# Optimization experiments

Measured on AMD Instinct MI355X. Metric: run time of the kernel, lower is better.

The kernel has to match this reference:

```python
import jax, jax.numpy as jnp
import numpy as np

DIM_MODEL = 1024
N_HEAD = 16
N_HEAD_H = 16
DIM_KEY = 64
DIM_VALUE = 64


def _linear_params(key, out_f, in_f):
    kw, kb = jax.random.split(key)
    bound = 1.0 / np.sqrt(in_f)
    W = jax.random.uniform(kw, (out_f, in_f), jnp.float32, -bound, bound)
    b = jax.random.uniform(kb, (out_f,), jnp.float32, -bound, bound)
    return W, b


def setup_inputs() -> dict:
    key = jax.random.key(0)
    ks = jax.random.split(key, 12)
    B, L = 4, 1024
    queries = jax.random.normal(ks[0], (B, L, DIM_MODEL), jnp.float32)
    keys = jax.random.normal(ks[1], (B, L, DIM_MODEL), jnp.float32)
    values = jax.random.normal(ks[2], (B, L, DIM_MODEL), jnp.float32)
    mask = jnp.ones((B, L), dtype=jnp.bool_)  # accepted but unused by the module
    attn_bias = jax.random.normal(ks[3], (B, N_HEAD, L), jnp.float32)
    Wq, bq = _linear_params(ks[4], DIM_KEY * N_HEAD, DIM_MODEL)
    Wk, bk = _linear_params(ks[5], DIM_KEY * N_HEAD, DIM_MODEL)
    Wv, bv = _linear_params(ks[6], DIM_VALUE * N_HEAD, DIM_MODEL)
    Wl, bl = _linear_params(ks[7], N_HEAD_H, N_HEAD)
    Ww, bw = _linear_params(ks[8], N_HEAD, N_HEAD_H)
    Wo, bo = _linear_params(ks[9], DIM_MODEL, DIM_VALUE * N_HEAD)
    return {
        "queries": queries, "keys": keys, "values": values,
        "mask": mask, "attn_bias": attn_bias,
        "Wq": Wq, "bq": bq, "Wk": Wk, "bk": bk, "Wv": Wv, "bv": bv,
        "Wl": Wl, "bl": bl, "Ww": Ww, "bw": bw, "Wo": Wo, "bo": bo,
    }


def reference(queries, keys, values, mask, attn_bias,
              Wq, bq, Wk, bk, Wv, bv, Wl, bl, Ww, bw, Wo, bo):
    B, Lq, _ = queries.shape
    # projections -> [B, L, H, d]
    q = (queries @ Wq.T + bq).reshape(B, Lq, N_HEAD, DIM_KEY)
    k = (keys @ Wk.T + bk).reshape(B, keys.shape[1], N_HEAD, DIM_KEY)
    v = (values @ Wv.T + bv).reshape(B, values.shape[1], N_HEAD, DIM_VALUE)
    scale = DIM_KEY ** (-0.5)
    # scores in the module's [B, Lq, Lk, H] layout (after its two transposes)
    scores = jnp.einsum("bqhd,bkhd->bqkh", scale * q, k)
    # attn_bias [B, H, Lq] -> [B, Lq, 1, H], broadcast over Lk
    scores = scores + jnp.transpose(attn_bias, (0, 2, 1))[:, :, None, :]
    # pre-softmax head mixing (fc_l): [B, Lq, Lk, H] -> [B, Lq, Lk, Hh]
    logits = jnp.einsum("bqkh,gh->bqkg", scores, Wl) + bl
    weights = jax.nn.softmax(logits, axis=2)  # softmax over Lk
    # post-softmax head mixing (fc_w): [B, Lq, Lk, Hh] -> [B, Lq, Lk, H]
    weights = jnp.einsum("bqkg,hg->bqkh", weights, Ww) + bw
    # weighted values: [B, Lq, H, dv] -> combine heads -> fc_o
    ctx = jnp.einsum("bqkh,bkhd->bqhd", weights, v).reshape(B, Lq, N_HEAD * DIM_VALUE)
    return ctx @ Wo.T + bo
```

## Files before the change

kernel.cpp:

```cpp
#include <hip/hip_runtime.h>

#define L_ 1024
#define DM 1024

typedef float f32x4 __attribute__((ext_vector_type(4)));
typedef _Float16 f16;
typedef _Float16 f16x8 __attribute__((ext_vector_type(8)));
typedef _Float16 f16x4 __attribute__((ext_vector_type(4)));

__device__ __forceinline__ void gload16(const void* g, void* l) {
  __builtin_amdgcn_global_load_lds(
      (const __attribute__((address_space(1))) unsigned int*)g,
      (__attribute__((address_space(3))) unsigned int*)l, 16, 0, 0);
}

__global__ __launch_bounds__(256) void cvt_all(const float* __restrict__ q,
    const float* __restrict__ k, const float* __restrict__ v,
    const float* __restrict__ wq, const float* __restrict__ wk,
    const float* __restrict__ wv, const float* __restrict__ wo,
    f16* __restrict__ dbig, f16* __restrict__ dw, f16* __restrict__ dwo) {
  int i = blockIdx.x * 256 + threadIdx.x;
  const float* s; f16* d; int off;
  if (i < 524288)       { s = q;  d = dbig;           off = i; }
  else if (i < 1048576) { s = k;  d = dbig + 4194304; off = i - 524288; }
  else if (i < 1572864) { s = v;  d = dbig + 8388608; off = i - 1048576; }
  else if (i < 1703936) { s = wq; d = dw;             off = i - 1572864; }
  else if (i < 1835008) { s = wk; d = dw + 1048576;   off = i - 1703936; }
  else if (i < 1966080) { s = wv; d = dw + 2097152;   off = i - 1835008; }
  else                  { s = wo; d = dwo;            off = i - 1966080; }
  const float4* sp = (const float4*)s + (size_t)off * 2;
  float4 a = sp[0], bb = sp[1];
  f16x8 o;
  o[0] = (f16)a.x;  o[1] = (f16)a.y;  o[2] = (f16)a.z;  o[3] = (f16)a.w;
  o[4] = (f16)bb.x; o[5] = (f16)bb.y; o[6] = (f16)bb.z; o[7] = (f16)bb.w;
  ((f16x8*)d)[off] = o;
}

__global__ __launch_bounds__(256) void biascat(const float* __restrict__ bq,
    const float* __restrict__ bk, const float* __restrict__ bv, float* __restrict__ o) {
  int t = blockIdx.x * 256 + threadIdx.x;
  o[t] = (t < 1024) ? bq[t] : (t < 2048) ? bk[t - 1024] : bv[t - 2048];
}

__global__ __launch_bounds__(256) void proj_gemm(const f16* __restrict__ Ain,
    const f16* __restrict__ Wc, const float* __restrict__ bcat, f16* __restrict__ QKVp) {
  alignas(16) __shared__ f16 At0[128 * 32];
  alignas(16) __shared__ f16 At1[128 * 32];
  alignas(16) __shared__ f16 Bt0[64 * 32];
  alignas(16) __shared__ f16 Bt1[64 * 32];
  int z = blockIdx.z;
  const f16* A = Ain + (size_t)z * 4194304;
  const f16* W = Wc + (size_t)z * 1048576;
  int t = threadIdx.x, lane = t & 63;
  int w = t >> 6, wr = w >> 1, wc = w & 1;
  int bid = blockIdx.x;
  int xcd = bid & 7, local = bid >> 3;
  int bm = (xcd * 4 + (local >> 4)) * 128;
  int bn = (local & 15) * 64;
  f32x4 acc[4][2] = {};
  int rbA = 32 * w + (lane >> 2);
  int rbB = 16 * w + (lane >> 2);
  int c8 = (lane & 3) * 8;
  const f16* gA = A + (size_t)(bm + rbA) * 1024 + c8;
  const f16* gB = W + (size_t)(bn + rbB) * 1024 + c8;
  f16* lA00 = &At0[(2 * w) * 512];      f16* lA01 = &At0[(2 * w + 1) * 512];
  f16* lA10 = &At1[(2 * w) * 512];      f16* lA11 = &At1[(2 * w + 1) * 512];
  f16* lB0  = &Bt0[w * 512];            f16* lB1  = &Bt1[w * 512];
  int ro = (lane & 15) * 32 + (lane >> 4) * 8;
  for (int kk = 0; kk < 1024; kk += 64) {
    gload16(gA + kk, lA00);
    gload16(gA + 16 * 1024 + kk, lA01);
    gload16(gA + kk + 32, lA10);
    gload16(gA + 16 * 1024 + kk + 32, lA11);
    gload16(gB + kk, lB0);
    gload16(gB + kk + 32, lB1);
    __syncthreads();
    f16x8 af[4], af2[4], bf[2], bf2[2];
    #pragma unroll
    for (int m = 0; m < 4; ++m) {
      af[m]  = *(const f16x8*)&At0[(wr * 64 + m * 16) * 32 + ro];
      af2[m] = *(const f16x8*)&At1[(wr * 64 + m * 16) * 32 + ro];
    }
    #pragma unroll
    for (int n = 0; n < 2; ++n) {
      bf[n]  = *(const f16x8*)&Bt0[(wc * 32 + n * 16) * 32 + ro];
      bf2[n] = *(const f16x8*)&Bt1[(wc * 32 + n * 16) * 32 + ro];
    }
    #pragma unroll
    for (int m = 0; m < 4; ++m)
      #pragma unroll
      for (int n = 0; n < 2; ++n) {
        acc[m][n] = __builtin_amdgcn_mfma_f32_16x16x32_f16(af[m], bf[n], acc[m][n], 0, 0, 0);
        acc[m][n] = __builtin_amdgcn_mfma_f32_16x16x32_f16(af2[m], bf2[n], acc[m][n], 0, 0, 0);
      }
    __syncthreads();
  }
  float scale = (z == 0) ? 0.125f : 1.0f;
  #pragma unroll
  for (int n = 0; n < 2; ++n) {
    int cn = bn + wc * 32 + n * 16 + (lane & 15);
    float bvv = bcat[z * 1024 + cn];
    #pragma unroll
    for (int m = 0; m < 4; ++m) {
      int r0 = bm + wr * 64 + m * 16 + (lane >> 4) * 4;
      #pragma unroll
      for (int r = 0; r < 4; ++r)
        QKVp[(size_t)(r0 + r) * 3072 + z * 1024 + cn] = (f16)((acc[m][n][r] + bvv) * scale);
    }
  }
}

__global__ __launch_bounds__(256) void gemm_out(const f16* __restrict__ A,
    const f16* __restrict__ W, const float* __restrict__ bias, float* __restrict__ C) {
  alignas(16) __shared__ f16 At0[128 * 32];
  alignas(16) __shared__ f16 At1[128 * 32];
  alignas(16) __shared__ f16 Bt0[64 * 32];
  alignas(16) __shared__ f16 Bt1[64 * 32];
  int t = threadIdx.x, lane = t & 63;
  int w = t >> 6, wr = w >> 1, wc = w & 1;
  int bid = blockIdx.x;
  int xcd = bid & 7, local = bid >> 3;
  int bm = (xcd * 4 + (local >> 4)) * 128;
  int bn = (local & 15) * 64;
  f32x4 acc[4][2] = {};
  int rbA = 32 * w + (lane >> 2);
  int rbB = 16 * w + (lane >> 2);
  int c8 = (lane & 3) * 8;
  const f16* gA = A + (size_t)(bm + rbA) * 1024 + c8;
  const f16* gB = W + (size_t)(bn + rbB) * 1024 + c8;
  f16* lA00 = &At0[(2 * w) * 512];      f16* lA01 = &At0[(2 * w + 1) * 512];
  f16* lA10 = &At1[(2 * w) * 512];      f16* lA11 = &At1[(2 * w + 1) * 512];
  f16* lB0  = &Bt0[w * 512];            f16* lB1  = &Bt1[w * 512];
  int ro = (lane & 15) * 32 + (lane >> 4) * 8;
  for (int kk = 0; kk < 1024; kk += 64) {
    gload16(gA + kk, lA00);
    gload16(gA + 16 * 1024 + kk, lA01);
    gload16(gA + kk + 32, lA10);
    gload16(gA + 16 * 1024 + kk + 32, lA11);
    gload16(gB + kk, lB0);
    gload16(gB + kk + 32, lB1);
    __syncthreads();
    f16x8 af[4], af2[4], bf[2], bf2[2];
    #pragma unroll
    for (int m = 0; m < 4; ++m) {
      af[m]  = *(const f16x8*)&At0[(wr * 64 + m * 16) * 32 + ro];
      af2[m] = *(const f16x8*)&At1[(wr * 64 + m * 16) * 32 + ro];
    }
    #pragma unroll
    for (int n = 0; n < 2; ++n) {
      bf[n]  = *(const f16x8*)&Bt0[(wc * 32 + n * 16) * 32 + ro];
      bf2[n] = *(const f16x8*)&Bt1[(wc * 32 + n * 16) * 32 + ro];
    }
    #pragma unroll
    for (int m = 0; m < 4; ++m)
      #pragma unroll
      for (int n = 0; n < 2; ++n) {
        acc[m][n] = __builtin_amdgcn_mfma_f32_16x16x32_f16(af[m], bf[n], acc[m][n], 0, 0, 0);
        acc[m][n] = __builtin_amdgcn_mfma_f32_16x16x32_f16(af2[m], bf2[n], acc[m][n], 0, 0, 0);
      }
    __syncthreads();
  }
  #pragma unroll
  for (int n = 0; n < 2; ++n) {
    int cn = bn + wc * 32 + n * 16 + (lane & 15);
    float bvv = bias[cn];
    #pragma unroll
    for (int m = 0; m < 4; ++m) {
      int r0 = bm + wr * 64 + m * 16 + (lane >> 4) * 4;
      #pragma unroll
      for (int r = 0; r < 4; ++r)
        C[(size_t)(r0 + r) * 1024 + cn] = acc[m][n][r] + bvv;
    }
  }
}

__global__ __launch_bounds__(256) void transpose_v(const f16* __restrict__ QKVp,
                                                   f16* __restrict__ Vt) {
  alignas(16) __shared__ f16 T[64 * 72];
  int bh = blockIdx.y;
  int b = bh >> 4, h = bh & 15;
  int kt = blockIdx.x;
  int t = threadIdx.x;
  int krow = t >> 2, part = t & 3;
  const f16x8* src = (const f16x8*)(QKVp + (size_t)(b * L_ + kt * 64 + krow) * 3072 + 2048 + h * 64 + part * 16);
  f16x8 v0 = src[0], v1 = src[1];
  *(f16x8*)&T[krow * 72 + part * 16] = v0;
  *(f16x8*)&T[krow * 72 + part * 16 + 8] = v1;
  __syncthreads();
  int drow = t >> 2;
  f16x8 o0, o1;
  #pragma unroll
  for (int j = 0; j < 8; ++j) o0[j] = T[(part * 16 + j) * 72 + drow];
  #pragma unroll
  for (int j = 0; j < 8; ++j) o1[j] = T[(part * 16 + 8 + j) * 72 + drow];
  f16* dst = Vt + (size_t)(bh * 64 + drow) * L_ + kt * 64 + part * 16;
  *(f16x8*)dst = o0;
  *(f16x8*)(dst + 8) = o1;
}

__global__ __launch_bounds__(256) void cbias_kernel(const float* __restrict__ ab,
    const float* __restrict__ Wl, const float* __restrict__ bl, float* __restrict__ cb) {
  int t = blockIdx.x * 256 + threadIdx.x;
  int b = t >> 14, q = (t >> 4) & 1023, g = t & 15;
  float s = bl[g];
  #pragma unroll
  for (int h = 0; h < 16; ++h) s += ab[(size_t)(b * 16 + h) * L_ + q] * Wl[g * 16 + h];
  cb[t] = s;
}

__global__ __launch_bounds__(256) void qk_gemm(const f16* __restrict__ QKVp,
                                               f16* __restrict__ S, int b0) {
  alignas(16) __shared__ f16 At[128 * 72];
  alignas(16) __shared__ f16 Bt[128 * 72];
  int t = threadIdx.x, lane = t & 63;
  int wid = t >> 6, wr = wid >> 1, wc = wid & 1;
  int kt = blockIdx.x, qt = blockIdx.y;
  int h = blockIdx.z & 15, bz = blockIdx.z >> 4;
  int b = b0 + bz;
  #pragma unroll
  for (int i = 0; i < 4; ++i) {
    int row = i * 32 + (t >> 3), c = (t & 7) * 8;
    *(f16x8*)&At[row * 72 + c] =
        *(const f16x8*)(QKVp + (size_t)(b * 1024 + qt * 128 + row) * 3072 + h * 64 + c);
    *(f16x8*)&Bt[row * 72 + c] =
        *(const f16x8*)(QKVp + (size_t)(b * 1024 + kt * 128 + row) * 3072 + 1024 + h * 64 + c);
  }
  __syncthreads();
  int l15 = lane & 15, lhi = lane >> 4;
  f32x4 acc[4][4] = {};
  #pragma unroll
  for (int s = 0; s < 2; ++s) {
    f16x8 af[4], bf[4];
    #pragma unroll
    for (int m = 0; m < 4; ++m) af[m] = *(const f16x8*)&At[(wr * 64 + m * 16 + l15) * 72 + s * 32 + lhi * 8];
    #pragma unroll
    for (int n = 0; n < 4; ++n) bf[n] = *(const f16x8*)&Bt[(wc * 64 + n * 16 + l15) * 72 + s * 32 + lhi * 8];
    #pragma unroll
    for (int m = 0; m < 4; ++m)
      #pragma unroll
      for (int n = 0; n < 4; ++n)
        acc[m][n] = __builtin_amdgcn_mfma_f32_16x16x32_f16(af[m], bf[n], acc[m][n], 0, 0, 0);
  }
  size_t Sh = (size_t)(bz * 16 + h) * 1048576;
  #pragma unroll
  for (int n = 0; n < 4; ++n) {
    int col = kt * 128 + wc * 64 + n * 16 + l15;
    #pragma unroll
    for (int m = 0; m < 4; ++m) {
      int q0 = qt * 128 + wr * 64 + m * 16 + lhi * 4;
      #pragma unroll
      for (int r = 0; r < 4; ++r)
        S[Sh + (size_t)(q0 + r) * 1024 + col] = (f16)acc[m][n][r];
    }
  }
}

__global__ __launch_bounds__(256) void msm_kernel(f16* __restrict__ S,
    const float* __restrict__ Wl, const float* __restrict__ Ww,
    const float* __restrict__ bwv, const float* __restrict__ cb, int b0) {
  alignas(16) __shared__ f16 Sl[16][1032];
  __shared__ float red[4][16];
  __shared__ float rlv16[16];
  int t = threadIdx.x;
  int q = blockIdx.x & 1023, bz = blockIdx.x >> 10;
  int lane = t & 63, w = t >> 6, l15 = lane & 15, lhi = lane >> 4;
  size_t Sq = (size_t)(bz * 16) * 1048576 + (size_t)q * 1024;
  #pragma unroll
  for (int i = 0; i < 8; ++i) {
    int idx = i * 256 + t, h = idx >> 7, c = (idx & 127) * 8;
    *(f16x8*)&Sl[h][c] = *(const f16x8*)(S + Sq + (size_t)h * 1048576 + c);
  }
  f16x4 b1;
  #pragma unroll
  for (int j = 0; j < 4; ++j) b1[j] = (f16)Wl[l15 * 16 + lhi * 4 + j];
  float cbv = cb[((size_t)((b0 + bz) * 1024 + q)) * 16 + l15];
  __syncthreads();
  float dsum = 0.f;
  for (int i = 0; i < 16; ++i) {
    int kt = w * 16 + i;
    int krow = kt * 16 + l15;
    f16x4 a1;
    #pragma unroll
    for (int j = 0; j < 4; ++j) a1[j] = Sl[lhi * 4 + j][krow];
    f32x4 d = __builtin_amdgcn_mfma_f32_16x16x16f16(a1, b1, (f32x4){0.f, 0.f, 0.f, 0.f}, 0, 0, 0);
    int k0 = kt * 16 + lhi * 4;
    f16x4 ev;
    #pragma unroll
    for (int r = 0; r < 4; ++r) {
      float e = __expf(d[r] + cbv);
      dsum += e;
      ev[r] = (f16)e;
    }
    *(f16x4*)&Sl[l15][k0] = ev;
  }
  dsum += __shfl_xor(dsum, 16);
  dsum += __shfl_xor(dsum, 32);
  if (lane < 16) red[w][lane] = dsum;
  __syncthreads();
  if (t < 16) rlv16[t] = 1.0f / (red[0][t] + red[1][t] + red[2][t] + red[3][t]);
  __syncthreads();
  f16x4 b2;
  #pragma unroll
  for (int j = 0; j < 4; ++j) b2[j] = (f16)(Ww[l15 * 16 + lhi * 4 + j] * rlv16[lhi * 4 + j]);
  float bwh = bwv[l15];
  for (int i = 0; i < 16; ++i) {
    int kt = w * 16 + i;
    int krow = kt * 16 + l15;
    f16x4 a2;
    #pragma unroll
    for (int j = 0; j < 4; ++j) a2[j] = Sl[lhi * 4 + j][krow];
    f32x4 d = __builtin_amdgcn_mfma_f32_16x16x16f16(a2, b2, (f32x4){0.f, 0.f, 0.f, 0.f}, 0, 0, 0);
    int k0 = kt * 16 + lhi * 4;
    f16x4 wv4;
    #pragma unroll
    for (int r = 0; r < 4; ++r) wv4[r] = (f16)(d[r] + bwh);
    *(f16x4*)&Sl[l15][k0] = wv4;
  }
  __syncthreads();
  #pragma unroll
  for (int i = 0; i < 8; ++i) {
    int idx = i * 256 + t, h = idx >> 7, c = (idx & 127) * 8;
    *(f16x8*)(S + Sq + (size_t)h * 1048576 + c) = *(f16x8*)&Sl[h][c];
  }
}

__global__ __launch_bounds__(256) void pv_gemm(const f16* __restrict__ Sw,
    const f16* __restrict__ Vt, f16* __restrict__ ctx, int b0) {
  alignas(16) __shared__ f16 Aw[32 * 72];
  alignas(16) __shared__ f16 Bv[64 * 72];
  int t = threadIdx.x, lane = t & 63, w = t >> 6;
  int qt = blockIdx.x, h = blockIdx.y, bz = blockIdx.z;
  int wr = w >> 1, wc = w & 1;
  int l15 = lane & 15, lhi = lane >> 4;
  const f16* Sh = Sw + (size_t)(bz * 16 + h) * 1048576 + (size_t)(qt * 32) * 1024;
  const f16* Vh = Vt + (size_t)((b0 + bz) * 16 + h) * 64 * 1024;
  f32x4 acc[2] = {};
  int srow = t >> 3, scol = (t & 7) * 8;
  for (int kk = 0; kk < 1024; kk += 64) {
    __syncthreads();
    *(f16x8*)&Aw[srow * 72 + scol] = *(const f16x8*)(Sh + (size_t)srow * 1024 + kk + scol);
    *(f16x8*)&Bv[srow * 72 + scol] = *(const f16x8*)(Vh + (size_t)srow * 1024 + kk + scol);
    *(f16x8*)&Bv[(srow + 32) * 72 + scol] = *(const f16x8*)(Vh + (size_t)(srow + 32) * 1024 + kk + scol);
    __syncthreads();
    #pragma unroll
    for (int s = 0; s < 2; ++s) {
      f16x8 af = *(const f16x8*)&Aw[(wr * 16 + l15) * 72 + s * 32 + lhi * 8];
      #pragma unroll
      for (int n = 0; n < 2; ++n) {
        f16x8 bf = *(const f16x8*)&Bv[(wc * 32 + n * 16 + l15) * 72 + s * 32 + lhi * 8];
        acc[n] = __builtin_amdgcn_mfma_f32_16x16x32_f16(af, bf, acc[n], 0, 0, 0);
      }
    }
  }
  #pragma unroll
  for (int n = 0; n < 2; ++n) {
    int col = h * 64 + wc * 32 + n * 16 + l15;
    int q0 = (b0 + bz) * 1024 + qt * 32 + wr * 16 + lhi * 4;
    #pragma unroll
    for (int r = 0; r < 4; ++r)
      ctx[(size_t)(q0 + r) * 1024 + col] = (f16)acc[n][r];
  }
}

extern "C" void kernel_launch(void* const* d_in, const int* in_sizes, int n_in,
                              void* d_out, int out_size, void* d_ws, size_t ws_size,
                              hipStream_t stream) {
  const float* queries = (const float*)d_in[0];
  const float* keys    = (const float*)d_in[1];
  const float* values  = (const float*)d_in[2];
  const float* ab  = (const float*)d_in[4];
  const float* Wq  = (const float*)d_in[5];  const float* bq = (const float*)d_in[6];
  const float* Wk  = (const float*)d_in[7];  const float* bk = (const float*)d_in[8];
  const float* Wv  = (const float*)d_in[9];  const float* bv = (const float*)d_in[10];
  const float* Wl  = (const float*)d_in[11]; const float* bl = (const float*)d_in[12];
  const float* Ww  = (const float*)d_in[13]; const float* bwp = (const float*)d_in[14];
  const float* Wo  = (const float*)d_in[15]; const float* bo = (const float*)d_in[16];

  char* ws = (char*)d_ws;
  const size_t MB = 1024 * 1024;
  bool full = ws_size >= 172 * MB;

  f16* qin   = (f16*)(ws + 0 * MB);
  f16* wqkv  = (f16*)(ws + 24 * MB);
  f16* S     = (f16*)(ws + 0 * MB);
  f16* QKVp  = (f16*)(ws + (full ? 128 : 32) * MB);
  f16* Vt    = (f16*)(ws + (full ? 152 : 56) * MB);
  float* cbp = (float*)(ws + (full ? 170 : 64) * MB);
  f16* wo16  = (f16*)(ws + (full ? 168 : 65) * MB);
  f16* ctx   = (f16*)(ws + (full ? 160 : 67) * MB);
  float* bqkv = (float*)(ws + (full ? 170 * MB + 512 * 1024 : 30 * MB));

  cvt_all<<<8192, 256, 0, stream>>>(queries, keys, values, Wq, Wk, Wv, Wo, qin, wqkv, wo16);
  biascat<<<12, 256, 0, stream>>>(bq, bk, bv, bqkv);
  proj_gemm<<<dim3(512, 1, 3), 256, 0, stream>>>(qin, wqkv, bqkv, QKVp);
  transpose_v<<<dim3(16, 64), 256, 0, stream>>>(QKVp, Vt);
  cbias_kernel<<<256, 256, 0, stream>>>(ab, Wl, bl, cbp);

  if (full) {
    qk_gemm<<<dim3(8, 8, 64), 256, 0, stream>>>(QKVp, S, 0);
    msm_kernel<<<4096, 256, 0, stream>>>(S, Wl, Ww, bwp, cbp, 0);
    pv_gemm<<<dim3(32, 16, 4), 256, 0, stream>>>(S, Vt, ctx, 0);
  } else {
    for (int b = 0; b < 4; ++b) {
      qk_gemm<<<dim3(8, 8, 16), 256, 0, stream>>>(QKVp, S, b);
      msm_kernel<<<1024, 256, 0, stream>>>(S, Wl, Ww, bwp, cbp, b);
      pv_gemm<<<dim3(32, 16, 1), 256, 0, stream>>>(S, Vt, ctx, b);
    }
  }

  gemm_out<<<dim3(512), 256, 0, stream>>>(ctx, wo16, bo, (float*)d_out);
}
```

Baseline: 196.4 us.

## Fuse fp32-to-fp16 activation conversion into the QKV projection GEMM

The standalone conversion of the query/key/value activations to fp16 is removed. The projection GEMM now reads the fp32 activations directly, converts them in registers and stores them into a padded LDS tile (row stride 36). This drops a full write and re-read of 24 MB of fp16 activations plus most of the conversion launch. In exchange each GEMM block reads twice the bytes per A tile through synchronous vector loads instead of async global-to-LDS loads, and those A loads are re-read by the 16 column blocks.

```diff
diff --git a/kernel.cpp b/kernel.cpp
--- a/kernel.cpp
+++ b/kernel.cpp
@@ -14,20 +14,15 @@
       (__attribute__((address_space(3))) unsigned int*)l, 16, 0, 0);
 }
 
-__global__ __launch_bounds__(256) void cvt_all(const float* __restrict__ q,
-    const float* __restrict__ k, const float* __restrict__ v,
-    const float* __restrict__ wq, const float* __restrict__ wk,
-    const float* __restrict__ wv, const float* __restrict__ wo,
-    f16* __restrict__ dbig, f16* __restrict__ dw, f16* __restrict__ dwo) {
+__global__ __launch_bounds__(256) void cvt_w(const float* __restrict__ wq,
+    const float* __restrict__ wk, const float* __restrict__ wv, const float* __restrict__ wo,
+    f16* __restrict__ dw, f16* __restrict__ dwo) {
   int i = blockIdx.x * 256 + threadIdx.x;
   const float* s; f16* d; int off;
-  if (i < 524288)       { s = q;  d = dbig;           off = i; }
-  else if (i < 1048576) { s = k;  d = dbig + 4194304; off = i - 524288; }
-  else if (i < 1572864) { s = v;  d = dbig + 8388608; off = i - 1048576; }
-  else if (i < 1703936) { s = wq; d = dw;             off = i - 1572864; }
-  else if (i < 1835008) { s = wk; d = dw + 1048576;   off = i - 1703936; }
-  else if (i < 1966080) { s = wv; d = dw + 2097152;   off = i - 1835008; }
-  else                  { s = wo; d = dwo;            off = i - 1966080; }
+  if (i < 131072)       { s = wq; d = dw;             off = i; }
+  else if (i < 262144)  { s = wk; d = dw + 1048576;   off = i - 131072; }
+  else if (i < 393216)  { s = wv; d = dw + 2097152;   off = i - 262144; }
+  else                  { s = wo; d = dwo;            off = i - 393216; }
   const float4* sp = (const float4*)s + (size_t)off * 2;
   float4 a = sp[0], bb = sp[1];
   f16x8 o;
@@ -42,14 +37,15 @@
   o[t] = (t < 1024) ? bq[t] : (t < 2048) ? bk[t - 1024] : bv[t - 2048];
 }
 
-__global__ __launch_bounds__(256) void proj_gemm(const f16* __restrict__ Ain,
+__global__ __launch_bounds__(256) void proj_gemm(const float* __restrict__ Aq,
+    const float* __restrict__ Ak, const float* __restrict__ Av,
     const f16* __restrict__ Wc, const float* __restrict__ bcat, f16* __restrict__ QKVp) {
-  alignas(16) __shared__ f16 At0[128 * 32];
-  alignas(16) __shared__ f16 At1[128 * 32];
+  alignas(16) __shared__ f16 At0[128 * 36];
+  alignas(16) __shared__ f16 At1[128 * 36];
   alignas(16) __shared__ f16 Bt0[64 * 32];
   alignas(16) __shared__ f16 Bt1[64 * 32];
   int z = blockIdx.z;
-  const f16* A = Ain + (size_t)z * 4194304;
+  const float* A = (z == 0) ? Aq : (z == 1) ? Ak : Av;
   const f16* W = Wc + (size_t)z * 1048576;
   int t = threadIdx.x, lane = t & 63;
   int w = t >> 6, wr = w >> 1, wc = w & 1;
@@ -58,33 +54,46 @@
   int bm = (xcd * 4 + (local >> 4)) * 128;
   int bn = (local & 15) * 64;
   f32x4 acc[4][2] = {};
-  int rbA = 32 * w + (lane >> 2);
+  int arow = t >> 1, ahalf = t & 1;
+  const float4* gA = (const float4*)(A + (size_t)(bm + arow) * 1024 + ahalf * 32);
+  f16* aDst = (ahalf ? At1 : At0) + arow * 36;
   int rbB = 16 * w + (lane >> 2);
   int c8 = (lane & 3) * 8;
-  const f16* gA = A + (size_t)(bm + rbA) * 1024 + c8;
   const f16* gB = W + (size_t)(bn + rbB) * 1024 + c8;
-  f16* lA00 = &At0[(2 * w) * 512];      f16* lA01 = &At0[(2 * w + 1) * 512];
-  f16* lA10 = &At1[(2 * w) * 512];      f16* lA11 = &At1[(2 * w + 1) * 512];
-  f16* lB0  = &Bt0[w * 512];            f16* lB1  = &Bt1[w * 512];
-  int ro = (lane & 15) * 32 + (lane >> 4) * 8;
+  f16* lB0 = &Bt0[w * 512];
+  f16* lB1 = &Bt1[w * 512];
+  int roA = (lane & 15) * 36 + (lane >> 4) * 8;
+  int roB = (lane & 15) * 32 + (lane >> 4) * 8;
   for (int kk = 0; kk < 1024; kk += 64) {
-    gload16(gA + kk, lA00);
-    gload16(gA + 16 * 1024 + kk, lA01);
-    gload16(gA + kk + 32, lA10);
-    gload16(gA + 16 * 1024 + kk + 32, lA11);
     gload16(gB + kk, lB0);
     gload16(gB + kk + 32, lB1);
+    const float4* ga = gA + (kk >> 2);
+    float4 v0 = ga[0], v1 = ga[1], v2 = ga[2], v3 = ga[3];
+    float4 v4 = ga[4], v5 = ga[5], v6 = ga[6], v7 = ga[7];
+    f16x8 o0, o1, o2, o3;
+    o0[0] = (f16)v0.x; o0[1] = (f16)v0.y; o0[2] = (f16)v0.z; o0[3] = (f16)v0.w;
+    o0[4] = (f16)v1.x; o0[5] = (f16)v1.y; o0[6] = (f16)v1.z; o0[7] = (f16)v1.w;
+    o1[0] = (f16)v2.x; o1[1] = (f16)v2.y; o1[2] = (f16)v2.z; o1[3] = (f16)v2.w;
+    o1[4] = (f16)v3.x; o1[5] = (f16)v3.y; o1[6] = (f16)v3.z; o1[7] = (f16)v3.w;
+    o2[0] = (f16)v4.x; o2[1] = (f16)v4.y; o2[2] = (f16)v4.z; o2[3] = (f16)v4.w;
+    o2[4] = (f16)v5.x; o2[5] = (f16)v5.y; o2[6] = (f16)v5.z; o2[7] = (f16)v5.w;
+    o3[0] = (f16)v6.x; o3[1] = (f16)v6.y; o3[2] = (f16)v6.z; o3[3] = (f16)v6.w;
+    o3[4] = (f16)v7.x; o3[5] = (f16)v7.y; o3[6] = (f16)v7.z; o3[7] = (f16)v7.w;
+    *(f16x8*)&aDst[0]  = o0;
+    *(f16x8*)&aDst[8]  = o1;
+    *(f16x8*)&aDst[16] = o2;
+    *(f16x8*)&aDst[24] = o3;
     __syncthreads();
     f16x8 af[4], af2[4], bf[2], bf2[2];
     #pragma unroll
     for (int m = 0; m < 4; ++m) {
-      af[m]  = *(const f16x8*)&At0[(wr * 64 + m * 16) * 32 + ro];
-      af2[m] = *(const f16x8*)&At1[(wr * 64 + m * 16) * 32 + ro];
+      af[m]  = *(const f16x8*)&At0[(wr * 64 + m * 16) * 36 + roA];
+      af2[m] = *(const f16x8*)&At1[(wr * 64 + m * 16) * 36 + roA];
     }
     #pragma unroll
     for (int n = 0; n < 2; ++n) {
-      bf[n]  = *(const f16x8*)&Bt0[(wc * 32 + n * 16) * 32 + ro];
-      bf2[n] = *(const f16x8*)&Bt1[(wc * 32 + n * 16) * 32 + ro];
+      bf[n]  = *(const f16x8*)&Bt0[(wc * 32 + n * 16) * 32 + roB];
+      bf2[n] = *(const f16x8*)&Bt1[(wc * 32 + n * 16) * 32 + roB];
     }
     #pragma unroll
     for (int m = 0; m < 4; ++m)
@@ -380,7 +389,6 @@
   const size_t MB = 1024 * 1024;
   bool full = ws_size >= 172 * MB;
 
-  f16* qin   = (f16*)(ws + 0 * MB);
   f16* wqkv  = (f16*)(ws + 24 * MB);
   f16* S     = (f16*)(ws + 0 * MB);
   f16* QKVp  = (f16*)(ws + (full ? 128 : 32) * MB);
@@ -390,9 +398,9 @@
   f16* ctx   = (f16*)(ws + (full ? 160 : 67) * MB);
   float* bqkv = (float*)(ws + (full ? 170 * MB + 512 * 1024 : 30 * MB));
 
-  cvt_all<<<8192, 256, 0, stream>>>(queries, keys, values, Wq, Wk, Wv, Wo, qin, wqkv, wo16);
+  cvt_w<<<2048, 256, 0, stream>>>(Wq, Wk, Wv, Wo, wqkv, wo16);
   biascat<<<12, 256, 0, stream>>>(bq, bk, bv, bqkv);
-  proj_gemm<<<dim3(512, 1, 3), 256, 0, stream>>>(qin, wqkv, bqkv, QKVp);
+  proj_gemm<<<dim3(512, 1, 3), 256, 0, stream>>>(queries, keys, values, wqkv, bqkv, QKVp);
   transpose_v<<<dim3(16, 64), 256, 0, stream>>>(QKVp, Vt);
   cbias_kernel<<<256, 256, 0, stream>>>(ab, Wl, bl, cbp);
 
```

New measurement: 258.2 us. 31.5% more time.
